# Performance work log

Measured on AMD Instinct MI355X. Metric: run time of the kernel, lower is better.

Reference implementation:

```python
import jax, jax.numpy as jnp
import numpy as np

N = 100000
E = 1600000
IN_C = 256
OUT_C = 128


def setup_inputs() -> dict:
    key = jax.random.key(0)
    k1, k2, k3 = jax.random.split(key, 3)
    x = jax.random.normal(k1, (N, IN_C), dtype=jnp.float32)
    edge_index = jax.random.randint(k2, (2, E), 0, N, dtype=jnp.int64)
    # Linear(in_channels, out_channels, bias=False): weight is [out, in]
    bound = 1.0 / np.sqrt(IN_C)
    weight = jax.random.uniform(k3, (OUT_C, IN_C), dtype=jnp.float32,
                                minval=-bound, maxval=bound)
    return {"x": x, "edge_index": edge_index, "weight": weight}


def reference(x, edge_index, weight):
    # Feature transform: x @ W.T  -> [N, OUT_C]
    h = x @ weight.T

    row, col = edge_index[0], edge_index[1]  # source, target

    # GCN normalization (add_self_loops=False, edge_weight=None -> ones)
    ones_e = jnp.ones((E,), dtype=h.dtype)
    deg = jax.ops.segment_sum(ones_e, col, num_segments=N)  # in-degree
    deg_inv_sqrt = jnp.where(deg > 0, jax.lax.rsqrt(deg), 0.0)
    ew = deg_inv_sqrt[row] * deg_inv_sqrt[col]  # [E]

    # Message passing: gather-multiply-scatter-add
    msgs = h[row] * ew[:, None]                       # [E, OUT_C]
    out = jax.ops.segment_sum(msgs, col, num_segments=N)  # [N, OUT_C]

    # Complex-to-real trick: negate second half, roll by half
    half = OUT_C // 2
    multiplier = jnp.concatenate([jnp.ones((half,), h.dtype),
                                  -jnp.ones((half,), h.dtype)])
    out = out * multiplier[None, :]
    out = jnp.roll(out, half, axis=-1)
    return out
```

## Files before the change

kernel.cpp:

```cpp
#include <hip/hip_runtime.h>
#include <hip/hip_bf16.h>

#define NN 100000
#define EE 1600000
#define INC 256
#define OUTC 128
#define NBUK 782
#define NPB  256
#define CHUNK ((EE + NPB - 1) / NPB)

typedef short bf16x8 __attribute__((ext_vector_type(8)));
typedef float f32x4 __attribute__((ext_vector_type(4)));

static __device__ __forceinline__ unsigned short f2bf(float f){
    unsigned u = __builtin_bit_cast(unsigned, f);
    u += 0x7fffu + ((u >> 16) & 1u);
    return (unsigned short)(u >> 16);
}
static __device__ __forceinline__ float bf2f(unsigned short h){
    unsigned u = ((unsigned)h) << 16;
    return __builtin_bit_cast(float, u);
}

__global__ void hist_kernel(const int* __restrict__ col, unsigned* __restrict__ bcnt){
    __shared__ unsigned h[NBUK];
    for (int i = threadIdx.x; i < NBUK; i += 256) h[i] = 0;
    __syncthreads();
    for (int i = blockIdx.x*blockDim.x + threadIdx.x; i < EE; i += gridDim.x*blockDim.x)
        atomicAdd(&h[((unsigned)col[i]) >> 7], 1u);
    __syncthreads();
    for (int i = threadIdx.x; i < NBUK; i += 256)
        if (h[i]) atomicAdd(&bcnt[i], h[i]);
}

__global__ void scanb_kernel(const unsigned* __restrict__ bcnt,
                             unsigned* __restrict__ base, unsigned* __restrict__ cursor){
    __shared__ unsigned tmp[1024];
    int t = threadIdx.x;
    unsigned v = (t < NBUK) ? bcnt[t] : 0u;
    tmp[t] = v;
    __syncthreads();
    for (int off = 1; off < 1024; off <<= 1){
        unsigned x = (t >= off) ? tmp[t-off] : 0u;
        __syncthreads();
        tmp[t] += x;
        __syncthreads();
    }
    if (t < NBUK){ unsigned ex = tmp[t] - v; base[t] = ex; cursor[t] = ex; }
    if (t == 0) base[NBUK] = EE;
}

__global__ void partition_kernel(const int* __restrict__ ei, unsigned* __restrict__ cursor,
                                 unsigned* __restrict__ packed){
    __shared__ unsigned cnt[NBUK], gpos[NBUK], cnt2[NBUK];
    int t = threadIdx.x;
    int s = blockIdx.x*CHUNK, e = min(s + CHUNK, EE);
    for (int i = t; i < NBUK; i += 256){ cnt[i] = 0; cnt2[i] = 0; }
    __syncthreads();
    for (int i = s + t; i < e; i += 256)
        atomicAdd(&cnt[((unsigned)ei[EE + i]) >> 7], 1u);
    __syncthreads();
    for (int i = t; i < NBUK; i += 256){
        unsigned c = cnt[i];
        gpos[i] = c ? atomicAdd(&cursor[i], c) : 0u;
    }
    __syncthreads();
    for (int i = s + t; i < e; i += 256){
        unsigned c = (unsigned)ei[EE + i];
        unsigned r = (unsigned)ei[i];
        unsigned b = c >> 7;
        unsigned rk = atomicAdd(&cnt2[b], 1u);
        packed[gpos[b] + rk] = ((c & 127u) << 24) | r;
    }
}

__global__ void sort_kernel(const unsigned* __restrict__ packed, const unsigned* __restrict__ base,
                            unsigned* __restrict__ erow, unsigned* __restrict__ noffs,
                            float* __restrict__ dinv){
    __shared__ unsigned cnt[128], cur[128], tmp[128];
    int t = threadIdx.x;
    unsigned s = base[blockIdx.x], e = base[blockIdx.x + 1];
    if (t < 128) cnt[t] = 0;
    __syncthreads();
    for (unsigned i = s + t; i < e; i += 256)
        atomicAdd(&cnt[packed[i] >> 24], 1u);
    __syncthreads();
    if (t < 128) tmp[t] = cnt[t];
    __syncthreads();
    for (int off = 1; off < 128; off <<= 1){
        unsigned v = (t >= off && t < 128) ? tmp[t-off] : 0u;
        __syncthreads();
        if (t < 128) tmp[t] += v;
        __syncthreads();
    }
    if (t < 128){
        unsigned ex = s + tmp[t] - cnt[t];
        cur[t] = ex;
        int node = blockIdx.x*128 + t;
        if (node < NN){
            noffs[node] = ex;
            dinv[node] = cnt[t] ? rsqrtf((float)cnt[t]) : 0.f;
        }
    }
    if (blockIdx.x == 0 && t == 0) noffs[NN] = EE;
    __syncthreads();
    for (unsigned i = s + t; i < e; i += 256){
        unsigned u = packed[i];
        unsigned pos = atomicAdd(&cur[u >> 24], 1u);
        erow[pos] = u & 0xFFFFFFu;
    }
}

__global__ void wprep_kernel(const float* __restrict__ w, unsigned short* __restrict__ wfrag){
    int idx = blockIdx.x*256 + threadIdx.x;
    if (idx < 8*8*64*8){
        int r = idx & 7, l = (idx >> 3) & 63, t = (idx >> 9) & 7, s = idx >> 12;
        int n = t*16 + (l & 15);
        int k = s*32 + ((l >> 4) << 3) + r;
        wfrag[idx] = f2bf(w[n*INC + k]);
    }
}

__launch_bounds__(256, 4)
__global__ void gemm_kernel(const float* __restrict__ x, const unsigned short* __restrict__ wfrag,
                            const float* __restrict__ dinv,
                            unsigned short* __restrict__ h2, int Nn){
    int tid = threadIdx.x;
    int wave = tid >> 6, lane = tid & 63;
    int mrow = blockIdx.x*64 + wave*16 + (lane & 15);
    const float* xr = x + (size_t)min(mrow, Nn-1) * INC;
    int kg = (lane >> 4) << 3;
    const bf16x8* wf = (const bf16x8*)wfrag;

    f32x4 acc[8];
    #pragma unroll
    for (int t = 0; t < 8; ++t) acc[t] = (f32x4){0.f,0.f,0.f,0.f};

    #pragma unroll
    for (int s = 0; s < 8; ++s){
        const float4* p = (const float4*)(xr + s*32 + kg);
        float4 a0 = p[0], a1 = p[1];
        bf16x8 af;
        af[0]=f2bf(a0.x); af[1]=f2bf(a0.y); af[2]=f2bf(a0.z); af[3]=f2bf(a0.w);
        af[4]=f2bf(a1.x); af[5]=f2bf(a1.y); af[6]=f2bf(a1.z); af[7]=f2bf(a1.w);
        #pragma unroll
        for (int t = 0; t < 8; ++t){
            bf16x8 bf = wf[(s*8 + t)*64 + lane];
            acc[t] = __builtin_amdgcn_mfma_f32_16x16x32_bf16(af, bf, acc[t], 0, 0, 0);
        }
    }

    int rbase = blockIdx.x*64 + wave*16 + ((lane >> 4) << 2);
    float sc[4];
    #pragma unroll
    for (int r = 0; r < 4; ++r){
        int row = rbase + r;
        sc[r] = (row < Nn) ? dinv[row] : 0.f;
    }
    #pragma unroll
    for (int t = 0; t < 8; ++t){
        int o  = t*16 + (lane & 15);
        int dc = (o + 64) & 127;
        float sgn = (o < 64) ? 1.f : -1.f;
        #pragma unroll
        for (int r = 0; r < 4; ++r){
            int row = rbase + r;
            if (row < Nn) h2[(size_t)row*OUTC + dc] = f2bf(sgn * sc[r] * acc[t][r]);
        }
    }
}

__launch_bounds__(256)
__global__ void gather_kernel(const unsigned short* __restrict__ h2,
                              const unsigned* __restrict__ noffs,
                              const unsigned* __restrict__ erow,
                              const float* __restrict__ dinv,
                              float* __restrict__ out, int Nn){
    int node = blockIdx.x*4 + (threadIdx.x >> 6);
    if (node >= Nn) return;
    int lane = threadIdx.x & 63;
    unsigned s = noffs[node], e = noffs[node+1];
    int half = lane >> 5;
    int cb = (lane & 31) << 2;

    float a0=0.f, a1=0.f, a2=0.f, a3=0.f;
    float b0=0.f, b1=0.f, b2=0.f, b3=0.f;
    unsigned p = s;
    for (; p + 4 <= e; p += 4){
        unsigned r0 = erow[p + half];
        unsigned r1 = erow[p + 2 + half];
        ushort4 v0 = *(const ushort4*)(h2 + (size_t)r0*OUTC + cb);
        ushort4 v1 = *(const ushort4*)(h2 + (size_t)r1*OUTC + cb);
        a0 += bf2f(v0.x); a1 += bf2f(v0.y); a2 += bf2f(v0.z); a3 += bf2f(v0.w);
        b0 += bf2f(v1.x); b1 += bf2f(v1.y); b2 += bf2f(v1.z); b3 += bf2f(v1.w);
    }
    for (; p < e; p += 2){
        unsigned idx = p + half;
        if (idx < e){
            unsigned row = erow[idx];
            ushort4 v = *(const ushort4*)(h2 + (size_t)row*OUTC + cb);
            a0 += bf2f(v.x); a1 += bf2f(v.y); a2 += bf2f(v.z); a3 += bf2f(v.w);
        }
    }
    a0 += b0; a1 += b1; a2 += b2; a3 += b3;
    a0 += __shfl_down(a0, 32);
    a1 += __shfl_down(a1, 32);
    a2 += __shfl_down(a2, 32);
    a3 += __shfl_down(a3, 32);
    if (half == 0){
        float wc = dinv[node];
        float4 o = {a0*wc, a1*wc, a2*wc, a3*wc};
        *(float4*)(out + (size_t)node*OUTC + cb) = o;
    }
}

extern "C" void kernel_launch(void* const* d_in, const int* in_sizes, int n_in,
                              void* d_out, int out_size, void* d_ws, size_t ws_size,
                              hipStream_t stream){
    const float* x  = (const float*)d_in[0];
    const int*   ei = (const int*)d_in[1];
    const float* w  = (const float*)d_in[2];
    float* out = (float*)d_out;

    char* ws = (char*)d_ws;
    size_t off = 0;
    auto alloc = [&](size_t b) -> char* {
        char* p = ws + off;
        off += (b + 255) & ~(size_t)255;
        return p;
    };
    unsigned* bcnt   = (unsigned*)alloc((size_t)NBUK*4);
    unsigned* base   = (unsigned*)alloc((size_t)(NBUK+1)*4);
    unsigned* cursor = (unsigned*)alloc((size_t)NBUK*4);
    float*    dinv   = (float*)  alloc((size_t)NN*4);
    unsigned* packed = (unsigned*)alloc((size_t)EE*4);
    unsigned* erow   = (unsigned*)alloc((size_t)EE*4);
    unsigned* noffs  = (unsigned*)alloc((size_t)(NN+1)*4);
    unsigned short* wfrag = (unsigned short*)alloc((size_t)8*8*64*8*2);
    unsigned short* h2 = (unsigned short*)alloc((size_t)NN*OUTC*2);

    hipMemsetAsync(bcnt, 0, (size_t)NBUK*4, stream);
    wprep_kernel<<<128, 256, 0, stream>>>(w, wfrag);
    hist_kernel<<<256, 256, 0, stream>>>(ei + EE, bcnt);
    scanb_kernel<<<1, 1024, 0, stream>>>(bcnt, base, cursor);
    partition_kernel<<<NPB, 256, 0, stream>>>(ei, cursor, packed);
    sort_kernel<<<NBUK, 256, 0, stream>>>(packed, base, erow, noffs, dinv);
    gemm_kernel<<<(NN+63)/64, 256, 0, stream>>>(x, wfrag, dinv, h2, NN);
    gather_kernel<<<(NN+3)/4, 256, 0, stream>>>(h2, noffs, erow, dinv, out, NN);
}
```

Baseline: 170.8 us.

## Slice h2 into column-major feature slices for L2-local gather

The GEMM now writes the transformed features in 8 column slices of 16 bf16 values, each slice stored contiguously across all nodes. The gather launches one block group per slice, so each block touches only a 3.2MB slice that fits in cache better. Edge indices are loaded cooperatively and broadcast with shuffles, and 8 lanes cover each 32-byte row segment so 8 edges are processed per wave step. The cost is that erow and noffs are read 8 times and each output write is a narrow 8-byte store.

```diff
diff --git a/kernel.cpp b/kernel.cpp
--- a/kernel.cpp
+++ b/kernel.cpp
@@ -8,6 +8,8 @@
 #define NBUK 782
 #define NPB  256
 #define CHUNK ((EE + NPB - 1) / NPB)
+#define NSL 8
+#define GNPB 16
 
 typedef short bf16x8 __attribute__((ext_vector_type(8)));
 typedef float f32x4 __attribute__((ext_vector_type(4)));
@@ -124,7 +126,7 @@
 __launch_bounds__(256, 4)
 __global__ void gemm_kernel(const float* __restrict__ x, const unsigned short* __restrict__ wfrag,
                             const float* __restrict__ dinv,
-                            unsigned short* __restrict__ h2, int Nn){
+                            unsigned short* __restrict__ h2s, int Nn){
     int tid = threadIdx.x;
     int wave = tid >> 6, lane = tid & 63;
     int mrow = blockIdx.x*64 + wave*16 + (lane & 15);
@@ -162,55 +164,73 @@
         int o  = t*16 + (lane & 15);
         int dc = (o + 64) & 127;
         float sgn = (o < 64) ? 1.f : -1.f;
+        int slice = dc >> 4, cis = dc & 15;
         #pragma unroll
         for (int r = 0; r < 4; ++r){
             int row = rbase + r;
-            if (row < Nn) h2[(size_t)row*OUTC + dc] = f2bf(sgn * sc[r] * acc[t][r]);
+            if (row < Nn)
+                h2s[((size_t)slice*NN + row)*16 + cis] = f2bf(sgn * sc[r] * acc[t][r]);
         }
     }
 }
 
 __launch_bounds__(256)
-__global__ void gather_kernel(const unsigned short* __restrict__ h2,
+__global__ void gather_kernel(const unsigned* __restrict__ h2su,
                               const unsigned* __restrict__ noffs,
                               const unsigned* __restrict__ erow,
                               const float* __restrict__ dinv,
-                              float* __restrict__ out, int Nn){
-    int node = blockIdx.x*4 + (threadIdx.x >> 6);
-    if (node >= Nn) return;
-    int lane = threadIdx.x & 63;
-    unsigned s = noffs[node], e = noffs[node+1];
-    int half = lane >> 5;
-    int cb = (lane & 31) << 2;
-
-    float a0=0.f, a1=0.f, a2=0.f, a3=0.f;
-    float b0=0.f, b1=0.f, b2=0.f, b3=0.f;
-    unsigned p = s;
-    for (; p + 4 <= e; p += 4){
-        unsigned r0 = erow[p + half];
-        unsigned r1 = erow[p + 2 + half];
-        ushort4 v0 = *(const ushort4*)(h2 + (size_t)r0*OUTC + cb);
-        ushort4 v1 = *(const ushort4*)(h2 + (size_t)r1*OUTC + cb);
-        a0 += bf2f(v0.x); a1 += bf2f(v0.y); a2 += bf2f(v0.z); a3 += bf2f(v0.w);
-        b0 += bf2f(v1.x); b1 += bf2f(v1.y); b2 += bf2f(v1.z); b3 += bf2f(v1.w);
-    }
-    for (; p < e; p += 2){
-        unsigned idx = p + half;
-        if (idx < e){
-            unsigned row = erow[idx];
-            ushort4 v = *(const ushort4*)(h2 + (size_t)row*OUTC + cb);
-            a0 += bf2f(v.x); a1 += bf2f(v.y); a2 += bf2f(v.z); a3 += bf2f(v.w);
-        }
-    }
-    a0 += b0; a1 += b1; a2 += b2; a3 += b3;
-    a0 += __shfl_down(a0, 32);
-    a1 += __shfl_down(a1, 32);
-    a2 += __shfl_down(a2, 32);
-    a3 += __shfl_down(a3, 32);
-    if (half == 0){
-        float wc = dinv[node];
-        float4 o = {a0*wc, a1*wc, a2*wc, a3*wc};
-        *(float4*)(out + (size_t)node*OUTC + cb) = o;
+                              float* __restrict__ out){
+    int slice = blockIdx.x & 7;
+    int nb = blockIdx.x >> 3;
+    int wave = threadIdx.x >> 6, lane = threadIdx.x & 63;
+    int g8 = lane >> 3;
+    int cp = lane & 7;
+    const unsigned* hs = h2su + (size_t)slice*NN*8;
+
+    for (int k = 0; k < 4; ++k){
+        int node = nb*GNPB + wave*4 + k;
+        if (node >= NN) break;
+        unsigned s = noffs[node], e = noffs[node+1];
+        unsigned deg = e - s;
+        float accL = 0.f, accH = 0.f;
+        for (unsigned b = 0; b < deg; b += 64){
+            unsigned my = b + lane;
+            unsigned eidx = (my < deg) ? erow[s + my] : 0u;
+            unsigned chunk = min(64u, deg - b);
+            unsigned j = 0;
+            for (; j + 16 <= chunk; j += 16){
+                unsigned r0 = __shfl(eidx, (int)(j + g8));
+                unsigned r1 = __shfl(eidx, (int)(j + 8 + g8));
+                unsigned v0 = hs[(size_t)r0*8 + cp];
+                unsigned v1 = hs[(size_t)r1*8 + cp];
+                accL += bf2f((unsigned short)(v0 & 0xFFFFu));
+                accH += bf2f((unsigned short)(v0 >> 16));
+                accL += bf2f((unsigned short)(v1 & 0xFFFFu));
+                accH += bf2f((unsigned short)(v1 >> 16));
+            }
+            if (j + 8 <= chunk){
+                unsigned r0 = __shfl(eidx, (int)(j + g8));
+                unsigned v0 = hs[(size_t)r0*8 + cp];
+                accL += bf2f((unsigned short)(v0 & 0xFFFFu));
+                accH += bf2f((unsigned short)(v0 >> 16));
+                j += 8;
+            }
+            unsigned jj = j + (unsigned)g8;
+            unsigned rr = __shfl(eidx, (int)(jj < chunk ? jj : chunk - 1));
+            if (jj < chunk){
+                unsigned v = hs[(size_t)rr*8 + cp];
+                accL += bf2f((unsigned short)(v & 0xFFFFu));
+                accH += bf2f((unsigned short)(v >> 16));
+            }
+        }
+        accL += __shfl_down(accL, 32); accH += __shfl_down(accH, 32);
+        accL += __shfl_down(accL, 16); accH += __shfl_down(accH, 16);
+        accL += __shfl_down(accL, 8);  accH += __shfl_down(accH, 8);
+        if (lane < 8){
+            float wc = dinv[node];
+            float2 o = {accL*wc, accH*wc};
+            *(float2*)(out + (size_t)node*OUTC + slice*16 + cp*2) = o;
+        }
     }
 }
 
@@ -237,7 +257,7 @@
     unsigned* erow   = (unsigned*)alloc((size_t)EE*4);
     unsigned* noffs  = (unsigned*)alloc((size_t)(NN+1)*4);
     unsigned short* wfrag = (unsigned short*)alloc((size_t)8*8*64*8*2);
-    unsigned short* h2 = (unsigned short*)alloc((size_t)NN*OUTC*2);
+    unsigned short* h2s = (unsigned short*)alloc((size_t)NN*OUTC*2);
 
     hipMemsetAsync(bcnt, 0, (size_t)NBUK*4, stream);
     wprep_kernel<<<128, 256, 0, stream>>>(w, wfrag);
@@ -245,6 +265,6 @@
     scanb_kernel<<<1, 1024, 0, stream>>>(bcnt, base, cursor);
     partition_kernel<<<NPB, 256, 0, stream>>>(ei, cursor, packed);
     sort_kernel<<<NBUK, 256, 0, stream>>>(packed, base, erow, noffs, dinv);
-    gemm_kernel<<<(NN+63)/64, 256, 0, stream>>>(x, wfrag, dinv, h2, NN);
-    gather_kernel<<<(NN+3)/4, 256, 0, stream>>>(h2, noffs, erow, dinv, out, NN);
-}
+    gemm_kernel<<<(NN+63)/64, 256, 0, stream>>>(x, wfrag, dinv, h2s, NN);
+    gather_kernel<<<((NN+GNPB-1)/GNPB)*NSL, 256, 0, stream>>>((const unsigned*)h2s, noffs, erow, dinv, out);
+}
```

Result: slower. 272.2 us (+59.4%).
